# Kernel optimization log

Hardware: AMD Instinct MI355X
Metric: run time of the kernel (lower is better)

## Reference

```python
import jax, jax.numpy as jnp
import numpy as np

N, D, B, K, DOUT = 100000, 128, 500000, 3, 128


def setup_inputs() -> dict:
    key = jax.random.key(0)
    k1, k2, k3 = jax.random.split(key, 3)
    x = jax.random.normal(k1, (N, D), dtype=jnp.float32)
    indices = jax.random.randint(k2, (B, K), 0, N, dtype=jnp.int64)
    # xavier_normal_ for weight [D*(K+1), DOUT]
    fan_in, fan_out = D * (K + 1), DOUT
    std = float(np.sqrt(2.0 / (fan_in + fan_out)))
    weight = jax.random.normal(k3, (fan_in, fan_out), dtype=jnp.float32) * std
    return {"x": x, "indices": indices, "weight": weight}


def reference(x, indices, weight):
    # _1_to_k, cfg='default', normalize=False
    # gather K node rows per hyperedge and concat: [B, K*D]
    x_nonpool = x[indices].reshape(indices.shape[0], -1)
    w_nonpool = weight[:-D]          # [K*D, DOUT]
    w_pool = weight[-D:]             # [D, DOUT]
    x_pool = jnp.sum(x, axis=0, keepdims=True)  # [1, D] (sum since normalize=False)
    return x_nonpool @ w_nonpool + x_pool @ w_pool  # [B, DOUT]
```

## Files before the change

kernel.cpp:

```cpp
#include <hip/hip_runtime.h>
#include <stdint.h>

#define NROWS 100000
#define DIMD  128
#define KKIDX 3
#define NDOUT 128
#define KDIM  384
#define NBAT  500000

typedef float  f4v  __attribute__((ext_vector_type(4)));
typedef short  s8v  __attribute__((ext_vector_type(8)));
typedef unsigned int u4v __attribute__((ext_vector_type(4)));

__device__ __forceinline__ short f2bf(float f) {
    union { float f; uint32_t u; } c; c.f = f;
    uint32_t u = c.u;
    uint32_t r = (u + 0x7FFFu + ((u >> 16) & 1u)) >> 16;
    return (short)r;
}

template<bool WRITE_BF>
__global__ void k_prep(const float* __restrict__ x, float* __restrict__ xpool_part,
                       unsigned short* __restrict__ xbf,
                       const float* __restrict__ w, unsigned short* __restrict__ wT) {
    if (blockIdx.x >= 400) {
        int b = blockIdx.x - 400;
        #pragma unroll
        for (int t = 0; t < 4; ++t) {
            int g = b * 1024 + t * 256 + threadIdx.x;
            int k = g >> 7;
            int n = g & 127;
            wT[n * KDIM + k] = (unsigned short)f2bf(w[g]);
        }
        return;
    }
    __shared__ float red[256];
    int col  = threadIdx.x & 127;
    int half = threadIdx.x >> 7;
    float acc = 0.f;
    int r0 = blockIdx.x * 250;
    for (int r = r0 + half; r < r0 + 250; r += 2) {
        float v = x[r * DIMD + col];
        acc += v;
        if (WRITE_BF) xbf[r * DIMD + col] = (unsigned short)f2bf(v);
    }
    red[threadIdx.x] = acc;
    __syncthreads();
    if (threadIdx.x < 128)
        xpool_part[blockIdx.x * 128 + threadIdx.x] = red[threadIdx.x] + red[threadIdx.x + 128];
}

__global__ void k_pool(const float* __restrict__ part, const float* __restrict__ w,
                       float* __restrict__ pool_out) {
    __shared__ float xp[128];
    int j = threadIdx.x;
    float s = 0.f;
    for (int b = 0; b < 400; ++b) s += part[b * 128 + j];
    xp[j] = s;
    __syncthreads();
    float acc = 0.f;
    for (int d = 0; d < DIMD; ++d)
        acc += xp[d] * w[(KDIM + d) * NDOUT + j];
    pool_out[j] = acc;
}

#define LSTR 200

template<bool XBF>
__global__ __launch_bounds__(512, 6)
void k_main(const float* __restrict__ x, const unsigned short* __restrict__ xbf,
            const int* __restrict__ idx, const unsigned short* __restrict__ wT,
            const float* __restrict__ pool, float* __restrict__ out) {
    __shared__ short wlds[128 * LSTR];
    const int tid  = threadIdx.x;
    const int wave = tid >> 6;
    const int lane = tid & 63;
    const int quad = lane >> 4;
    const int l16  = lane & 15;

    const int rowg = wave >> 1;
    const int cbase = (wave & 1) * 64;
    const int rowb = blockIdx.x * 128 + rowg * 32;

    int goff[2][KKIDX];
    #pragma unroll
    for (int mt = 0; mt < 2; ++mt) {
        int r = rowb + mt * 16 + l16;
        if (r >= NBAT) r = NBAT - 1;
        #pragma unroll
        for (int s = 0; s < KKIDX; ++s)
            goff[mt][s] = idx[r * 3 + s] * DIMD;
    }

    f4v acc[2][4];
    #pragma unroll
    for (int mt = 0; mt < 2; ++mt)
        #pragma unroll
        for (int nt = 0; nt < 4; ++nt) {
            f4v z = {0.f, 0.f, 0.f, 0.f};
            acc[mt][nt] = z;
        }

    const int sn   = tid >> 2;
    const int sseg = tid & 3;

    s8v aC[2];
    #pragma unroll
    for (int mt = 0; mt < 2; ++mt) {
        if (XBF) {
            aC[mt] = *(const s8v*)(xbf + goff[mt][0] + quad * 8);
        } else {
            const float* ap = x + goff[mt][0] + quad * 8;
            f4v v0 = *(const f4v*)ap;
            f4v v1 = *(const f4v*)(ap + 4);
            s8v a;
            a[0] = f2bf(v0[0]); a[1] = f2bf(v0[1]);
            a[2] = f2bf(v0[2]); a[3] = f2bf(v0[3]);
            a[4] = f2bf(v1[0]); a[5] = f2bf(v1[1]);
            a[6] = f2bf(v1[2]); a[7] = f2bf(v1[3]);
            aC[mt] = a;
        }
    }

    #pragma unroll
    for (int p = 0; p < 2; ++p) {
        __syncthreads();
        #pragma unroll
        for (int j = 0; j < 6; ++j) {
            int k = sseg * 48 + j * 8;
            *(u4v*)(&wlds[sn * LSTR + k]) = *(const u4v*)(wT + sn * KDIM + p * 192 + k);
        }
        __syncthreads();

        #pragma unroll
        for (int ks = 0; ks < 6; ++ks) {
            const int kstep = p * 6 + ks;

            s8v aN[2];
            if (kstep < 11) {
                const int kn   = kstep + 1;
                const int srci = kn >> 2;
                const int colb = (kn & 3) * 32 + quad * 8;
                #pragma unroll
                for (int mt = 0; mt < 2; ++mt) {
                    if (XBF) {
                        aN[mt] = *(const s8v*)(xbf + goff[mt][srci] + colb);
                    } else {
                        const float* ap = x + goff[mt][srci] + colb;
                        f4v v0 = *(const f4v*)ap;
                        f4v v1 = *(const f4v*)(ap + 4);
                        s8v a;
                        a[0] = f2bf(v0[0]); a[1] = f2bf(v0[1]);
                        a[2] = f2bf(v0[2]); a[3] = f2bf(v0[3]);
                        a[4] = f2bf(v1[0]); a[5] = f2bf(v1[1]);
                        a[6] = f2bf(v1[2]); a[7] = f2bf(v1[3]);
                        aN[mt] = a;
                    }
                }
            }

            const int krow = ks * 32 + quad * 8;
            s8v bF[4];
            #pragma unroll
            for (int nt = 0; nt < 4; ++nt)
                bF[nt] = *(const s8v*)(&wlds[(cbase + nt * 16 + l16) * LSTR + krow]);
            #pragma unroll
            for (int mt = 0; mt < 2; ++mt)
                #pragma unroll
                for (int nt = 0; nt < 4; ++nt)
                    acc[mt][nt] = __builtin_amdgcn_mfma_f32_16x16x32_bf16(
                        bF[nt], aC[mt], acc[mt][nt], 0, 0, 0);

            if (kstep < 11) { aC[0] = aN[0]; aC[1] = aN[1]; }
        }
    }

    #pragma unroll
    for (int nt = 0; nt < 4; ++nt) {
        f4v pv = *(const f4v*)(pool + cbase + nt * 16 + quad * 4);
        #pragma unroll
        for (int mt = 0; mt < 2; ++mt) {
            int r = rowb + mt * 16 + l16;
            if (r < NBAT) {
                f4v v = acc[mt][nt] + pv;
                __builtin_nontemporal_store(v,
                    (f4v*)(out + (size_t)r * NDOUT + cbase + nt * 16 + quad * 4));
            }
        }
    }
}

extern "C" void kernel_launch(void* const* d_in, const int* in_sizes, int n_in,
                              void* d_out, int out_size, void* d_ws, size_t ws_size,
                              hipStream_t stream) {
    const float* x   = (const float*)d_in[0];
    const int*   idx = (const int*)d_in[1];
    const float* w   = (const float*)d_in[2];
    float*       out = (float*)d_out;

    char* ws = (char*)d_ws;
    float* pool_out        = (float*)ws;
    float* xpool_part      = (float*)(ws + 512);
    unsigned short* wT     = (unsigned short*)(ws + 205312);
    unsigned short* xbf    = (unsigned short*)(ws + 303616);
    const size_t NEED_BIG  = 303616 + (size_t)NROWS * DIMD * 2;
    const bool big = ws_size >= NEED_BIG;

    if (big) k_prep<true ><<<448, 256, 0, stream>>>(x, xpool_part, xbf, w, wT);
    else     k_prep<false><<<448, 256, 0, stream>>>(x, xpool_part, xbf, w, wT);
    k_pool<<<1, 128, 0, stream>>>(xpool_part, w, pool_out);

    const int grid = (NBAT + 127) / 128;
    if (big) k_main<true ><<<grid, 512, 0, stream>>>(x, xbf, idx, wT, pool_out, out);
    else     k_main<false><<<grid, 512, 0, stream>>>(x, xbf, idx, wT, pool_out, out);
}
```

Before: 515.3 us.

## Give each wave full output width and prefetch whole gathered rows per phase

```diff
diff --git a/kernel.cpp b/kernel.cpp
--- a/kernel.cpp
+++ b/kernel.cpp
@@ -64,10 +64,28 @@
     pool_out[j] = acc;
 }
 
-#define LSTR 200
+template<bool XBF_>
+__device__ __forceinline__ s8v load_frag(const float* __restrict__ x,
+                                         const unsigned short* __restrict__ xbf, int off) {
+    if (XBF_) {
+        return *(const s8v*)(xbf + off);
+    } else {
+        const float* ap = x + off;
+        f4v v0 = *(const f4v*)ap;
+        f4v v1 = *(const f4v*)(ap + 4);
+        s8v a;
+        a[0] = f2bf(v0[0]); a[1] = f2bf(v0[1]);
+        a[2] = f2bf(v0[2]); a[3] = f2bf(v0[3]);
+        a[4] = f2bf(v1[0]); a[5] = f2bf(v1[1]);
+        a[6] = f2bf(v1[2]); a[7] = f2bf(v1[3]);
+        return a;
+    }
+}
+
+#define LSTR 136
 
 template<bool XBF>
-__global__ __launch_bounds__(512, 6)
+__global__ __launch_bounds__(256, 3)
 void k_main(const float* __restrict__ x, const unsigned short* __restrict__ xbf,
             const int* __restrict__ idx, const unsigned short* __restrict__ wT,
             const float* __restrict__ pool, float* __restrict__ out) {
@@ -78,9 +96,7 @@
     const int quad = lane >> 4;
     const int l16  = lane & 15;
 
-    const int rowg = wave >> 1;
-    const int cbase = (wave & 1) * 64;
-    const int rowb = blockIdx.x * 128 + rowg * 32;
+    const int rowb = blockIdx.x * 128 + wave * 32;
 
     int goff[2][KKIDX];
     #pragma unroll
@@ -92,99 +108,76 @@
             goff[mt][s] = idx[r * 3 + s] * DIMD;
     }
 
-    f4v acc[2][4];
+    f4v acc[2][8];
     #pragma unroll
     for (int mt = 0; mt < 2; ++mt)
         #pragma unroll
-        for (int nt = 0; nt < 4; ++nt) {
+        for (int nt = 0; nt < 8; ++nt) {
             f4v z = {0.f, 0.f, 0.f, 0.f};
             acc[mt][nt] = z;
         }
 
-    const int sn   = tid >> 2;
-    const int sseg = tid & 3;
-
-    s8v aC[2];
-    #pragma unroll
-    for (int mt = 0; mt < 2; ++mt) {
-        if (XBF) {
-            aC[mt] = *(const s8v*)(xbf + goff[mt][0] + quad * 8);
-        } else {
-            const float* ap = x + goff[mt][0] + quad * 8;
-            f4v v0 = *(const f4v*)ap;
-            f4v v1 = *(const f4v*)(ap + 4);
-            s8v a;
-            a[0] = f2bf(v0[0]); a[1] = f2bf(v0[1]);
-            a[2] = f2bf(v0[2]); a[3] = f2bf(v0[3]);
-            a[4] = f2bf(v1[0]); a[5] = f2bf(v1[1]);
-            a[6] = f2bf(v1[2]); a[7] = f2bf(v1[3]);
-            aC[mt] = a;
-        }
-    }
-
-    #pragma unroll
-    for (int p = 0; p < 2; ++p) {
-        __syncthreads();
-        #pragma unroll
-        for (int j = 0; j < 6; ++j) {
-            int k = sseg * 48 + j * 8;
-            *(u4v*)(&wlds[sn * LSTR + k]) = *(const u4v*)(wT + sn * KDIM + p * 192 + k);
-        }
-        __syncthreads();
-
-        #pragma unroll
-        for (int ks = 0; ks < 6; ++ks) {
-            const int kstep = p * 6 + ks;
-
-            s8v aN[2];
-            if (kstep < 11) {
-                const int kn   = kstep + 1;
-                const int srci = kn >> 2;
-                const int colb = (kn & 3) * 32 + quad * 8;
-                #pragma unroll
-                for (int mt = 0; mt < 2; ++mt) {
-                    if (XBF) {
-                        aN[mt] = *(const s8v*)(xbf + goff[mt][srci] + colb);
-                    } else {
-                        const float* ap = x + goff[mt][srci] + colb;
-                        f4v v0 = *(const f4v*)ap;
-                        f4v v1 = *(const f4v*)(ap + 4);
-                        s8v a;
-                        a[0] = f2bf(v0[0]); a[1] = f2bf(v0[1]);
-                        a[2] = f2bf(v0[2]); a[3] = f2bf(v0[3]);
-                        a[4] = f2bf(v1[0]); a[5] = f2bf(v1[1]);
-                        a[6] = f2bf(v1[2]); a[7] = f2bf(v1[3]);
-                        aN[mt] = a;
-                    }
-                }
-            }
-
-            const int krow = ks * 32 + quad * 8;
-            s8v bF[4];
-            #pragma unroll
-            for (int nt = 0; nt < 4; ++nt)
-                bF[nt] = *(const s8v*)(&wlds[(cbase + nt * 16 + l16) * LSTR + krow]);
-            #pragma unroll
-            for (int mt = 0; mt < 2; ++mt)
-                #pragma unroll
-                for (int nt = 0; nt < 4; ++nt)
-                    acc[mt][nt] = __builtin_amdgcn_mfma_f32_16x16x32_bf16(
-                        bF[nt], aC[mt], acc[mt][nt], 0, 0, 0);
-
-            if (kstep < 11) { aC[0] = aN[0]; aC[1] = aN[1]; }
-        }
-    }
-
-    #pragma unroll
-    for (int nt = 0; nt < 4; ++nt) {
-        f4v pv = *(const f4v*)(pool + cbase + nt * 16 + quad * 4);
+    const int sn = tid >> 1;
+    const int sh = tid & 1;
+    const unsigned short* wsrc = wT + sn * KDIM + sh * 64;
+    short* wdst = &wlds[sn * LSTR + sh * 64];
+
+    s8v aA[2][4], aB[2][4];
+    #pragma unroll
+    for (int mt = 0; mt < 2; ++mt)
+        #pragma unroll
+        for (int kk = 0; kk < 4; ++kk)
+            aA[mt][kk] = load_frag<XBF>(x, xbf, goff[mt][0] + kk * 32 + quad * 8);
+
+#define DO_PHASE(R, CUR, NXT, DO_PF, PFROW)                                     \
+    {                                                                           \
+        __syncthreads();                                                        \
+        _Pragma("unroll")                                                       \
+        for (int j = 0; j < 8; ++j)                                             \
+            *(u4v*)(wdst + j * 8) = *(const u4v*)(wsrc + (R) * 128 + j * 8);    \
+        __syncthreads();                                                        \
+        if (DO_PF) {                                                            \
+            _Pragma("unroll")                                                   \
+            for (int mt = 0; mt < 2; ++mt)                                      \
+                _Pragma("unroll")                                               \
+                for (int kk = 0; kk < 4; ++kk)                                  \
+                    NXT[mt][kk] = load_frag<XBF>(x, xbf,                        \
+                        goff[mt][PFROW] + kk * 32 + quad * 8);                  \
+        }                                                                       \
+        _Pragma("unroll")                                                       \
+        for (int kk = 0; kk < 4; ++kk) {                                        \
+            const int krow = kk * 32 + quad * 8;                                \
+            _Pragma("unroll")                                                   \
+            for (int h = 0; h < 2; ++h) {                                       \
+                s8v bF[4];                                                      \
+                _Pragma("unroll")                                               \
+                for (int q = 0; q < 4; ++q)                                     \
+                    bF[q] = *(const s8v*)(&wlds[((h * 4 + q) * 16 + l16) * LSTR + krow]); \
+                _Pragma("unroll")                                               \
+                for (int mt = 0; mt < 2; ++mt)                                  \
+                    _Pragma("unroll")                                           \
+                    for (int q = 0; q < 4; ++q)                                 \
+                        acc[mt][h * 4 + q] = __builtin_amdgcn_mfma_f32_16x16x32_bf16( \
+                            bF[q], CUR[mt][kk], acc[mt][h * 4 + q], 0, 0, 0);   \
+            }                                                                   \
+        }                                                                       \
+    }
+
+    DO_PHASE(0, aA, aB, 1, 1)
+    DO_PHASE(1, aB, aA, 1, 2)
+    DO_PHASE(2, aA, aB, 0, 0)
+#undef DO_PHASE
+
+    #pragma unroll
+    for (int nt = 0; nt < 8; ++nt) {
+        f4v pv = *(const f4v*)(pool + nt * 16 + quad * 4);
         #pragma unroll
         for (int mt = 0; mt < 2; ++mt) {
             int r = rowb + mt * 16 + l16;
             if (r < NBAT) {
                 f4v v = acc[mt][nt] + pv;
                 __builtin_nontemporal_store(v,
-                    (f4v*)(out + (size_t)r * NDOUT + cbase + nt * 16 + quad * 4));
+                    (f4v*)(out + (size_t)r * NDOUT + nt * 16 + quad * 4));
             }
         }
     }
@@ -211,6 +204,6 @@
     k_pool<<<1, 128, 0, stream>>>(xpool_part, w, pool_out);
 
     const int grid = (NBAT + 127) / 128;
-    if (big) k_main<true ><<<grid, 512, 0, stream>>>(x, xbf, idx, wT, pool_out, out);
-    else     k_main<false><<<grid, 512, 0, stream>>>(x, xbf, idx, wT, pool_out, out);
-}
+    if (big) k_main<true ><<<grid, 256, 0, stream>>>(x, xbf, idx, wT, pool_out, out);
+    else     k_main<false><<<grid, 256, 0, stream>>>(x, xbf, idx, wT, pool_out, out);
+}
```

After: 473.2 us. 1.09x faster.

## Precompute per-node projections then gather-and-sum instead of per-hyperedge GEMM

Applied to the files above, without the earlier changes.

```diff
diff --git a/kernel.cpp b/kernel.cpp
--- a/kernel.cpp
+++ b/kernel.cpp
@@ -10,7 +10,7 @@
 
 typedef float  f4v  __attribute__((ext_vector_type(4)));
 typedef short  s8v  __attribute__((ext_vector_type(8)));
-typedef unsigned int u4v __attribute__((ext_vector_type(4)));
+typedef short  s4v  __attribute__((ext_vector_type(4)));
 
 __device__ __forceinline__ short f2bf(float f) {
     union { float f; uint32_t u; } c; c.f = f;
@@ -18,11 +18,21 @@
     uint32_t r = (u + 0x7FFFu + ((u >> 16) & 1u)) >> 16;
     return (short)r;
 }
-
-template<bool WRITE_BF>
+__device__ __forceinline__ float bf2f(unsigned short h) {
+    union { uint32_t u; float f; } c; c.u = ((uint32_t)h) << 16;
+    return c.f;
+}
+__device__ __forceinline__ s8v cvt8(const float* __restrict__ p) {
+    f4v v0 = *(const f4v*)p;
+    f4v v1 = *(const f4v*)(p + 4);
+    s8v a;
+    a[0] = f2bf(v0[0]); a[1] = f2bf(v0[1]); a[2] = f2bf(v0[2]); a[3] = f2bf(v0[3]);
+    a[4] = f2bf(v1[0]); a[5] = f2bf(v1[1]); a[6] = f2bf(v1[2]); a[7] = f2bf(v1[3]);
+    return a;
+}
+
 __global__ void k_prep(const float* __restrict__ x, float* __restrict__ xpool_part,
-                       unsigned short* __restrict__ xbf,
-                       const float* __restrict__ w, unsigned short* __restrict__ wT) {
+                       const float* __restrict__ w, unsigned short* __restrict__ wT2) {
     if (blockIdx.x >= 400) {
         int b = blockIdx.x - 400;
         #pragma unroll
@@ -30,7 +40,8 @@
             int g = b * 1024 + t * 256 + threadIdx.x;
             int k = g >> 7;
             int n = g & 127;
-            wT[n * KDIM + k] = (unsigned short)f2bf(w[g]);
+            int s = k >> 7, d = k & 127;
+            wT2[(s * 128 + n) * 128 + d] = (unsigned short)f2bf(w[g]);
         }
         return;
     }
@@ -39,11 +50,8 @@
     int half = threadIdx.x >> 7;
     float acc = 0.f;
     int r0 = blockIdx.x * 250;
-    for (int r = r0 + half; r < r0 + 250; r += 2) {
-        float v = x[r * DIMD + col];
-        acc += v;
-        if (WRITE_BF) xbf[r * DIMD + col] = (unsigned short)f2bf(v);
-    }
+    for (int r = r0 + half; r < r0 + 250; r += 2)
+        acc += x[r * DIMD + col];
     red[threadIdx.x] = acc;
     __syncthreads();
     if (threadIdx.x < 128)
@@ -64,130 +72,126 @@
     pool_out[j] = acc;
 }
 
-#define LSTR 200
-
-template<bool XBF>
-__global__ __launch_bounds__(512, 6)
-void k_main(const float* __restrict__ x, const unsigned short* __restrict__ xbf,
-            const int* __restrict__ idx, const unsigned short* __restrict__ wT,
-            const float* __restrict__ pool, float* __restrict__ out) {
-    __shared__ short wlds[128 * LSTR];
+__global__ __launch_bounds__(256, 4)
+void k_zgemm(const float* __restrict__ x, const unsigned short* __restrict__ wT2,
+             unsigned short* __restrict__ zbf) {
     const int tid  = threadIdx.x;
     const int wave = tid >> 6;
     const int lane = tid & 63;
     const int quad = lane >> 4;
     const int l16  = lane & 15;
-
-    const int rowg = wave >> 1;
-    const int cbase = (wave & 1) * 64;
-    const int rowb = blockIdx.x * 128 + rowg * 32;
-
-    int goff[2][KKIDX];
-    #pragma unroll
-    for (int mt = 0; mt < 2; ++mt) {
-        int r = rowb + mt * 16 + l16;
-        if (r >= NBAT) r = NBAT - 1;
-        #pragma unroll
-        for (int s = 0; s < KKIDX; ++s)
-            goff[mt][s] = idx[r * 3 + s] * DIMD;
-    }
-
-    f4v acc[2][4];
+    const int rowb  = blockIdx.x * 32;
+    const int jbase = wave * 96;
+
+    f4v acc[2][6];
     #pragma unroll
     for (int mt = 0; mt < 2; ++mt)
         #pragma unroll
-        for (int nt = 0; nt < 4; ++nt) {
+        for (int nt = 0; nt < 6; ++nt) {
             f4v z = {0.f, 0.f, 0.f, 0.f};
             acc[mt][nt] = z;
         }
 
-    const int sn   = tid >> 2;
-    const int sseg = tid & 3;
-
-    s8v aC[2];
-    #pragma unroll
-    for (int mt = 0; mt < 2; ++mt) {
-        if (XBF) {
-            aC[mt] = *(const s8v*)(xbf + goff[mt][0] + quad * 8);
-        } else {
-            const float* ap = x + goff[mt][0] + quad * 8;
-            f4v v0 = *(const f4v*)ap;
-            f4v v1 = *(const f4v*)(ap + 4);
-            s8v a;
-            a[0] = f2bf(v0[0]); a[1] = f2bf(v0[1]);
-            a[2] = f2bf(v0[2]); a[3] = f2bf(v0[3]);
-            a[4] = f2bf(v1[0]); a[5] = f2bf(v1[1]);
-            a[6] = f2bf(v1[2]); a[7] = f2bf(v1[3]);
-            aC[mt] = a;
-        }
-    }
-
-    #pragma unroll
-    for (int p = 0; p < 2; ++p) {
-        __syncthreads();
-        #pragma unroll
-        for (int j = 0; j < 6; ++j) {
-            int k = sseg * 48 + j * 8;
-            *(u4v*)(&wlds[sn * LSTR + k]) = *(const u4v*)(wT + sn * KDIM + p * 192 + k);
-        }
-        __syncthreads();
-
-        #pragma unroll
-        for (int ks = 0; ks < 6; ++ks) {
-            const int kstep = p * 6 + ks;
-
-            s8v aN[2];
-            if (kstep < 11) {
-                const int kn   = kstep + 1;
-                const int srci = kn >> 2;
-                const int colb = (kn & 3) * 32 + quad * 8;
-                #pragma unroll
-                for (int mt = 0; mt < 2; ++mt) {
-                    if (XBF) {
-                        aN[mt] = *(const s8v*)(xbf + goff[mt][srci] + colb);
-                    } else {
-                        const float* ap = x + goff[mt][srci] + colb;
-                        f4v v0 = *(const f4v*)ap;
-                        f4v v1 = *(const f4v*)(ap + 4);
-                        s8v a;
-                        a[0] = f2bf(v0[0]); a[1] = f2bf(v0[1]);
-                        a[2] = f2bf(v0[2]); a[3] = f2bf(v0[3]);
-                        a[4] = f2bf(v1[0]); a[5] = f2bf(v1[1]);
-                        a[6] = f2bf(v1[2]); a[7] = f2bf(v1[3]);
-                        aN[mt] = a;
-                    }
-                }
-            }
-
-            const int krow = ks * 32 + quad * 8;
-            s8v bF[4];
-            #pragma unroll
-            for (int nt = 0; nt < 4; ++nt)
-                bF[nt] = *(const s8v*)(&wlds[(cbase + nt * 16 + l16) * LSTR + krow]);
-            #pragma unroll
-            for (int mt = 0; mt < 2; ++mt)
-                #pragma unroll
-                for (int nt = 0; nt < 4; ++nt)
-                    acc[mt][nt] = __builtin_amdgcn_mfma_f32_16x16x32_bf16(
-                        bF[nt], aC[mt], acc[mt][nt], 0, 0, 0);
-
-            if (kstep < 11) { aC[0] = aN[0]; aC[1] = aN[1]; }
-        }
-    }
-
-    #pragma unroll
-    for (int nt = 0; nt < 4; ++nt) {
-        f4v pv = *(const f4v*)(pool + cbase + nt * 16 + quad * 4);
+    const float* xr0 = x + (rowb + l16) * DIMD;
+    const float* xr1 = x + (rowb + 16 + l16) * DIMD;
+
+    #pragma unroll
+    for (int kk = 0; kk < 4; ++kk) {
+        const int cb = kk * 32 + quad * 8;
+        s8v aF0 = cvt8(xr0 + cb);
+        s8v aF1 = cvt8(xr1 + cb);
+        #pragma unroll
+        for (int nt = 0; nt < 6; ++nt) {
+            s8v bF = *(const s8v*)(wT2 + (jbase + nt * 16 + l16) * DIMD + cb);
+            acc[0][nt] = __builtin_amdgcn_mfma_f32_16x16x32_bf16(bF, aF0, acc[0][nt], 0, 0, 0);
+            acc[1][nt] = __builtin_amdgcn_mfma_f32_16x16x32_bf16(bF, aF1, acc[1][nt], 0, 0, 0);
+        }
+    }
+
+    #pragma unroll
+    for (int nt = 0; nt < 6; ++nt)
         #pragma unroll
         for (int mt = 0; mt < 2; ++mt) {
             int r = rowb + mt * 16 + l16;
-            if (r < NBAT) {
-                f4v v = acc[mt][nt] + pv;
-                __builtin_nontemporal_store(v,
-                    (f4v*)(out + (size_t)r * NDOUT + cbase + nt * 16 + quad * 4));
+            int c = jbase + nt * 16 + quad * 4;
+            s4v v;
+            v[0] = f2bf(acc[mt][nt][0]); v[1] = f2bf(acc[mt][nt][1]);
+            v[2] = f2bf(acc[mt][nt][2]); v[3] = f2bf(acc[mt][nt][3]);
+            *(s4v*)(zbf + r * KDIM + c) = v;
+        }
+}
+
+__global__ __launch_bounds__(256, 6)
+void k_scatter(const int* __restrict__ idx, const unsigned short* __restrict__ zbf,
+               const float* __restrict__ pool, float* __restrict__ out) {
+    const int tid  = threadIdx.x;
+    const int l16  = tid & 15;
+    const int rgrp = tid >> 4;
+    const int c0   = l16 * 8;
+    f4v pv0 = *(const f4v*)(pool + c0);
+    f4v pv1 = *(const f4v*)(pool + c0 + 4);
+    const int stride = gridDim.x * 16;
+
+    for (int r = blockIdx.x * 16 + rgrp; r < NBAT; r += 2 * stride) {
+        const int r2 = r + stride;
+        const bool has2 = (r2 < NBAT);
+
+        int i0 = idx[r * 3 + 0], i1 = idx[r * 3 + 1], i2 = idx[r * 3 + 2];
+        s8v z0 = *(const s8v*)(zbf + i0 * KDIM +   0 + c0);
+        s8v z1 = *(const s8v*)(zbf + i1 * KDIM + 128 + c0);
+        s8v z2 = *(const s8v*)(zbf + i2 * KDIM + 256 + c0);
+
+        s8v y0 = z0, y1 = z0, y2 = z0;
+        int q0 = 0, q1 = 0, q2 = 0;
+        if (has2) {
+            q0 = idx[r2 * 3 + 0]; q1 = idx[r2 * 3 + 1]; q2 = idx[r2 * 3 + 2];
+            y0 = *(const s8v*)(zbf + q0 * KDIM +   0 + c0);
+            y1 = *(const s8v*)(zbf + q1 * KDIM + 128 + c0);
+            y2 = *(const s8v*)(zbf + q2 * KDIM + 256 + c0);
+        }
+
+        f4v o0 = pv0, o1 = pv1;
+        #pragma unroll
+        for (int e = 0; e < 4; ++e) {
+            o0[e] += bf2f((unsigned short)z0[e])     + bf2f((unsigned short)z1[e])
+                   + bf2f((unsigned short)z2[e]);
+            o1[e] += bf2f((unsigned short)z0[e + 4]) + bf2f((unsigned short)z1[e + 4])
+                   + bf2f((unsigned short)z2[e + 4]);
+        }
+        float* op = out + (size_t)r * NDOUT + c0;
+        __builtin_nontemporal_store(o0, (f4v*)op);
+        __builtin_nontemporal_store(o1, (f4v*)(op + 4));
+
+        if (has2) {
+            f4v p0 = pv0, p1 = pv1;
+            #pragma unroll
+            for (int e = 0; e < 4; ++e) {
+                p0[e] += bf2f((unsigned short)y0[e])     + bf2f((unsigned short)y1[e])
+                       + bf2f((unsigned short)y2[e]);
+                p1[e] += bf2f((unsigned short)y0[e + 4]) + bf2f((unsigned short)y1[e + 4])
+                       + bf2f((unsigned short)y2[e + 4]);
             }
-        }
-    }
+            float* op2 = out + (size_t)r2 * NDOUT + c0;
+            __builtin_nontemporal_store(p0, (f4v*)op2);
+            __builtin_nontemporal_store(p1, (f4v*)(op2 + 4));
+        }
+    }
+}
+
+__global__ void k_fb(const float* __restrict__ x, const int* __restrict__ idx,
+                     const float* __restrict__ w, const float* __restrict__ pool,
+                     float* __restrict__ out) {
+    int b = blockIdx.x;
+    int j = threadIdx.x;
+    float acc = pool[j];
+    #pragma unroll
+    for (int s = 0; s < KKIDX; ++s) {
+        int ir = idx[b * 3 + s];
+        const float* xr = x + ir * DIMD;
+        for (int d = 0; d < DIMD; ++d)
+            acc += xr[d] * w[(s * 128 + d) * NDOUT + j];
+    }
+    out[(size_t)b * NDOUT + j] = acc;
 }
 
 extern "C" void kernel_launch(void* const* d_in, const int* in_sizes, int n_in,
@@ -201,16 +205,18 @@
     char* ws = (char*)d_ws;
     float* pool_out        = (float*)ws;
     float* xpool_part      = (float*)(ws + 512);
-    unsigned short* wT     = (unsigned short*)(ws + 205312);
-    unsigned short* xbf    = (unsigned short*)(ws + 303616);
-    const size_t NEED_BIG  = 303616 + (size_t)NROWS * DIMD * 2;
-    const bool big = ws_size >= NEED_BIG;
-
-    if (big) k_prep<true ><<<448, 256, 0, stream>>>(x, xpool_part, xbf, w, wT);
-    else     k_prep<false><<<448, 256, 0, stream>>>(x, xpool_part, xbf, w, wT);
-    k_pool<<<1, 128, 0, stream>>>(xpool_part, w, pool_out);
-
-    const int grid = (NBAT + 127) / 128;
-    if (big) k_main<true ><<<grid, 512, 0, stream>>>(x, xbf, idx, wT, pool_out, out);
-    else     k_main<false><<<grid, 512, 0, stream>>>(x, xbf, idx, wT, pool_out, out);
-}
+    unsigned short* wT2    = (unsigned short*)(ws + 205312);
+    unsigned short* zbf    = (unsigned short*)(ws + 303616);
+    const size_t NEED      = 303616 + (size_t)NROWS * KDIM * 2;
+
+    if (ws_size >= NEED) {
+        k_prep <<<448, 256, 0, stream>>>(x, xpool_part, w, wT2);
+        k_zgemm<<<3125, 256, 0, stream>>>(x, wT2, zbf);
+        k_pool <<<1, 128, 0, stream>>>(xpool_part, w, pool_out);
+        k_scatter<<<2048, 256, 0, stream>>>(idx, zbf, pool_out, out);
+    } else {
+        k_prep <<<400, 256, 0, stream>>>(x, xpool_part, w, wT2);
+        k_pool <<<1, 128, 0, stream>>>(xpool_part, w, pool_out);
+        k_fb   <<<NBAT, 128, 0, stream>>>(x, idx, w, pool_out, out);
+    }
+}
```

Result: faster. 478.8 us (-7.1%).
